# Performance work log

Hardware: AMD Instinct MI355X
Metric: run time of the kernel (lower is better)

Reference implementation:

```python
import jax, jax.numpy as jnp
import numpy as np

KSIZE = 51  # radius=50 is even -> incremented to 51 in __init__


def _gaussian_1d(ksize):
    # cv2.getGaussianKernel with sigma<=0: sigma = 0.3*((ksize-1)*0.5 - 1) + 0.8
    sigma = 0.3 * ((ksize - 1) * 0.5 - 1) + 0.8
    x = np.arange(ksize, dtype=np.float64) - (ksize - 1) / 2
    g = np.exp(-(x * x) / (2.0 * sigma * sigma))
    g = g / g.sum()
    return g.astype(np.float32)


def _blur(img, kernel1d):
    """Separable Gaussian blur with reflect padding.
    Mathematically identical to the 2D conv with outer(g, g) in the torch code.
    img: (b, c, h, w), kernel1d: (k,)
    """
    k = kernel1d.shape[0]
    p = k // 2
    b, c, h, w = img.shape
    x = jnp.pad(img, ((0, 0), (0, 0), (p, p), (p, p)), mode='reflect')
    x = x.reshape(b * c, 1, h + 2 * p, w + 2 * p)
    # vertical pass then horizontal pass (conv vs correlation irrelevant: symmetric kernel)
    kv = kernel1d.reshape(1, 1, k, 1)
    kh = kernel1d.reshape(1, 1, 1, k)
    dn = ('NCHW', 'OIHW', 'NCHW')
    x = jax.lax.conv_general_dilated(x, kv, (1, 1), 'VALID', dimension_numbers=dn)
    x = jax.lax.conv_general_dilated(x, kh, (1, 1), 'VALID', dimension_numbers=dn)
    return x.reshape(b, c, h, w)


def setup_inputs() -> dict:
    key = jax.random.key(0)
    img = jax.random.uniform(key, (16, 3, 512, 512), dtype=jnp.float32)
    kernel1d = jnp.asarray(_gaussian_1d(KSIZE))
    return {"img": img, "kernel1d": kernel1d}


def reference(img, kernel1d):
    weight = 0.5
    threshold = 10.0
    blur = _blur(img, kernel1d)
    residual = img - blur
    mask = (jnp.abs(residual) * 255.0 > threshold).astype(img.dtype)
    soft_mask = _blur(mask, kernel1d)
    sharp = jnp.clip(img + weight * residual, 0.0, 1.0)
    return soft_mask * sharp + (1.0 - soft_mask) * img
```

## Files before the change

kernel.cpp:

```cpp
#include <hip/hip_runtime.h>
#include <hip/hip_bf16.h>


typedef __attribute__((ext_vector_type(8))) short bf16x8;
typedef __attribute__((ext_vector_type(4))) float f32x4;

constexpr int IMG = 512, NIMG = 48, K = 51;
constexpr int SP = 136;
constexpr int YP = 136;
constexpr int SROWS = 128;
constexpr int SDATA = 122;

__device__ __forceinline__ float bf2f(unsigned short u) {
    return __builtin_bit_cast(float, (unsigned)u << 16);
}
__device__ __forceinline__ unsigned short f2bf(float f) {
    unsigned u = __builtin_bit_cast(unsigned, f);
    u += 0x7FFF + ((u >> 16) & 1);
    return (unsigned short)(u >> 16);
}
__device__ __forceinline__ int refl(int i) {
    i = i < 0 ? -i : i;
    return i >= IMG ? 2 * IMG - 2 - i : i;
}

template <int PASS>
__global__ __launch_bounds__(512, 6) void usm_kern(const float* __restrict__ img,
                                                   unsigned short* __restrict__ resbuf,
                                                   float* __restrict__ out,
                                                   const float* __restrict__ k1d) {
    __shared__ unsigned short st[SROWS * SP];
    __shared__ unsigned short Hl[64 * YP];

    const int tid = threadIdx.x, lane = tid & 63;
    const int wv = __builtin_amdgcn_readfirstlane(tid >> 6);
    const int m16 = lane & 15, g = lane >> 4;

    const int id = blockIdx.x;
    const int sw = (id & 7) * 384 + (id >> 3);
    const int bz = sw >> 6, r6 = sw & 63, byy = r6 >> 3, bxx = r6 & 7;
    const int x0 = bxx * 64, y0 = byy * 64;
    const size_t base = (size_t)bz * (IMG * IMG);

#pragma unroll
    for (int e = 0; e < 4; ++e) {
        const int idx = tid + e * 512;
        const int band = idx >> 10, rem = idx & 1023;
        const int mm = rem >> 6, kk = rem & 63;
        const int t = kk - mm + band;
        Hl[idx] = ((unsigned)t < (unsigned)K) ? f2bf(k1d[t]) : (unsigned short)0;
    }

    const bool xedge = (bxx == 0) | (bxx == 7);
    const int r0 = tid >> 4, c8 = (tid & 15) * 8;
#pragma unroll
    for (int j = 0; j < 4; ++j) {
        const int s = r0 + 32 * j;
        const int y = refl(y0 - 33 + min(s, SDATA - 1));
        const size_t rowb = base + (size_t)y * IMG;
        unsigned pk[4];
        if (PASS == 0) {
            float v[8];
            if (!xedge) {
                const f32x4 f0 = *(const f32x4*)&img[rowb + (x0 - 32 + c8)];
                const f32x4 f1 = *(const f32x4*)&img[rowb + (x0 - 32 + c8 + 4)];
#pragma unroll
                for (int e2 = 0; e2 < 4; ++e2) { v[e2] = f0[e2]; v[e2 + 4] = f1[e2]; }
            } else {
#pragma unroll
                for (int e2 = 0; e2 < 8; ++e2) v[e2] = img[rowb + refl(x0 - 32 + c8 + e2)];
            }
#pragma unroll
            for (int w = 0; w < 4; ++w)
                pk[w] = (unsigned)f2bf(v[2 * w]) | ((unsigned)f2bf(v[2 * w + 1]) << 16);
        } else {
            unsigned short u[8];
            if (!xedge) {
                const uint4 q4 = *(const uint4*)&resbuf[rowb + (x0 - 32 + c8)];
                const unsigned ww[4] = {q4.x, q4.y, q4.z, q4.w};
#pragma unroll
                for (int w = 0; w < 4; ++w) {
                    u[2 * w] = (unsigned short)ww[w];
                    u[2 * w + 1] = (unsigned short)(ww[w] >> 16);
                }
            } else {
#pragma unroll
                for (int e2 = 0; e2 < 8; ++e2) u[e2] = resbuf[rowb + refl(x0 - 32 + c8 + e2)];
            }
#pragma unroll
            for (int w = 0; w < 4; ++w) {
                const unsigned lo = ((u[2 * w]     & 0x7FFFu) > 0x3D20u) ? 0x3F80u : 0u;
                const unsigned hi = ((u[2 * w + 1] & 0x7FFFu) > 0x3D20u) ? 0x3F80u : 0u;
                pk[w] = lo | (hi << 16);
            }
        }
        *(uint4*)&st[s * SP + c8] = make_uint4(pk[0], pk[1], pk[2], pk[3]);
    }
    __syncthreads();

    bf16x8 a_v[2], a_h[2];
#pragma unroll
    for (int rs = 0; rs < 2; ++rs) {
        a_v[rs] = *(const bf16x8*)&Hl[m16 * 64 + rs * 32 + 8 * g];
        a_h[rs] = *(const bf16x8*)&Hl[1024 + m16 * 64 + rs * 32 + 8 * g];
    }
    const float gg0 = k1d[0], gg49 = k1d[49], gg50 = k1d[50];
    __syncthreads();

#pragma unroll
    for (int k4 = 0; k4 < 4; ++k4) {
        const int t = wv + 8 * k4;
        const int xs = t & 3, yt = t >> 2;
        const int n = 16 * yt + m16;
        f32x4 acc = {0.f, 0.f, 0.f, 0.f};
#pragma unroll
        for (int rs = 0; rs < 2; ++rs) {
            const bf16x8 b = *(const bf16x8*)&st[n * SP + 16 * xs + 8 + 32 * rs + 8 * g];
            acc = __builtin_amdgcn_mfma_f32_16x16x32_bf16(a_h[rs], b, acc, 0, 0, 0);
        }
        if (g == 0) acc[0] = fmaf(gg0,  bf2f(st[n * SP + 16 * xs + 7]),  acc[0]);
        if (g == 3) acc[3] = fmaf(gg50, bf2f(st[n * SP + 16 * xs + 72]), acc[3]);
#pragma unroll
        for (int q = 0; q < 4; ++q)
            Hl[(16 * xs + 4 * g + q) * YP + n] = f2bf(acc[q]);
    }
    __syncthreads();

#pragma unroll
    for (int k2 = 0; k2 < 2; ++k2) {
        const int t = wv + 8 * k2;
        const int xs2 = t & 3, ys = t >> 2;
        const int xl = 16 * xs2 + m16;
        f32x4 acc = {0.f, 0.f, 0.f, 0.f};
#pragma unroll
        for (int rs = 0; rs < 2; ++rs) {
            const bf16x8 b = *(const bf16x8*)&Hl[xl * YP + 16 * ys + 8 + 32 * rs + 8 * g];
            acc = __builtin_amdgcn_mfma_f32_16x16x32_bf16(a_v[rs], b, acc, 0, 0, 0);
        }
        if (g == 3) {
            const float h72 = bf2f(Hl[xl * YP + 16 * ys + 72]);
            const float h73 = bf2f(Hl[xl * YP + 16 * ys + 73]);
            acc[2] = fmaf(gg50, h72, acc[2]);
            acc[3] = fmaf(gg49, h72, fmaf(gg50, h73, acc[3]));
        }
        const int yl0 = 16 * ys + 4 * g;
#pragma unroll
        for (int q = 0; q < 4; ++q) {
            const size_t di = base + (size_t)(y0 + yl0 + q) * IMG + (x0 + xl);
            const float iv = img[di];
            if (PASS == 0) {
                resbuf[di] = f2bf(iv - acc[q]);
            } else {
                const float rv = bf2f(resbuf[di]);
                float sharp = fmaf(0.5f, rv, iv);
                sharp = fminf(fmaxf(sharp, 0.f), 1.f);
                out[di] = fmaf(acc[q], sharp - iv, iv);
            }
        }
    }
}

extern "C" void kernel_launch(void* const* d_in, const int* in_sizes, int n_in,
                              void* d_out, int out_size, void* d_ws, size_t ws_size,
                              hipStream_t stream) {
    (void)in_sizes; (void)n_in; (void)out_size; (void)ws_size;
    const float* img = (const float*)d_in[0];
    const float* k1d = (const float*)d_in[1];
    float* out = (float*)d_out;
    unsigned short* rs = (unsigned short*)d_ws;

    const dim3 grid(NIMG * 64);

    usm_kern<0><<<grid, 512, 0, stream>>>(img, rs, out, k1d);
    usm_kern<1><<<grid, 512, 0, stream>>>(img, rs, out, k1d);
}
```

Measured before the change: 103.6 us.

## Store byte mask in pass 0, build MFMA kernel fragments in registers

Pass 0 now computes the threshold mask from the fp32 residual and writes it as a separate byte buffer. Pass 1 reads that byte mask for its halo-heavy tile load instead of re-reading the bf16 residual and thresholding it. The banded Gaussian A-fragments are built directly in registers from k1d rather than staged through shared memory, which removes one barrier, and addressing switches to 32-bit offsets from per-image base pointers. The cost is an extra byte store per pixel in pass 0, and the mask now comes from the unrounded residual, so it can differ slightly from the old bf16-based threshold.

After: 98.33 us. 1.05x faster.

```diff
diff --git a/kernel.cpp b/kernel.cpp
--- a/kernel.cpp
+++ b/kernel.cpp
@@ -27,6 +27,7 @@
 template <int PASS>
 __global__ __launch_bounds__(512, 6) void usm_kern(const float* __restrict__ img,
                                                    unsigned short* __restrict__ resbuf,
+                                                   unsigned char* __restrict__ maskbuf,
                                                    float* __restrict__ out,
                                                    const float* __restrict__ k1d) {
     __shared__ unsigned short st[SROWS * SP];
@@ -41,70 +42,70 @@
     const int bz = sw >> 6, r6 = sw & 63, byy = r6 >> 3, bxx = r6 & 7;
     const int x0 = bxx * 64, y0 = byy * 64;
     const size_t base = (size_t)bz * (IMG * IMG);
+    const float* __restrict__ imgb = img + base;
+    unsigned short* __restrict__ resb = resbuf + base;
+    unsigned char* __restrict__ maskb = maskbuf + base;
+    float* __restrict__ outb = out + base;
 
+    bf16x8 a_v[2], a_h[2];
 #pragma unroll
-    for (int e = 0; e < 4; ++e) {
-        const int idx = tid + e * 512;
-        const int band = idx >> 10, rem = idx & 1023;
-        const int mm = rem >> 6, kk = rem & 63;
-        const int t = kk - mm + band;
-        Hl[idx] = ((unsigned)t < (unsigned)K) ? f2bf(k1d[t]) : (unsigned short)0;
+    for (int rs = 0; rs < 2; ++rs) {
+        float gt[9];
+#pragma unroll
+        for (int e = 0; e < 9; ++e) {
+            const int t = 32 * rs + 8 * g + e - m16;
+            gt[e] = ((unsigned)t < (unsigned)K) ? k1d[t] : 0.f;
+        }
+#pragma unroll
+        for (int j = 0; j < 8; ++j) {
+            a_v[rs][j] = (short)f2bf(gt[j]);
+            a_h[rs][j] = (short)f2bf(gt[j + 1]);
+        }
     }
+    const float gg0 = k1d[0], gg49 = k1d[49], gg50 = k1d[50];
 
     const bool xedge = (bxx == 0) | (bxx == 7);
-    const int r0 = tid >> 4, c8 = (tid & 15) * 8;
+    const int r0t = tid >> 4, c8 = (tid & 15) * 8;
 #pragma unroll
     for (int j = 0; j < 4; ++j) {
-        const int s = r0 + 32 * j;
-        const int y = refl(y0 - 33 + min(s, SDATA - 1));
-        const size_t rowb = base + (size_t)y * IMG;
+        const int s = r0t + 32 * j;
+        const int rowo = refl(y0 - 33 + min(s, SDATA - 1)) * IMG + (x0 - 32 + c8);
         unsigned pk[4];
         if (PASS == 0) {
             float v[8];
             if (!xedge) {
-                const f32x4 f0 = *(const f32x4*)&img[rowb + (x0 - 32 + c8)];
-                const f32x4 f1 = *(const f32x4*)&img[rowb + (x0 - 32 + c8 + 4)];
+                const f32x4 f0 = *(const f32x4*)&imgb[rowo];
+                const f32x4 f1 = *(const f32x4*)&imgb[rowo + 4];
 #pragma unroll
-                for (int e2 = 0; e2 < 4; ++e2) { v[e2] = f0[e2]; v[e2 + 4] = f1[e2]; }
+                for (int e = 0; e < 4; ++e) { v[e] = f0[e]; v[e + 4] = f1[e]; }
             } else {
+                const int rb = rowo - (x0 - 32 + c8);
 #pragma unroll
-                for (int e2 = 0; e2 < 8; ++e2) v[e2] = img[rowb + refl(x0 - 32 + c8 + e2)];
+                for (int e = 0; e < 8; ++e) v[e] = imgb[rb + refl(x0 - 32 + c8 + e)];
             }
 #pragma unroll
             for (int w = 0; w < 4; ++w)
                 pk[w] = (unsigned)f2bf(v[2 * w]) | ((unsigned)f2bf(v[2 * w + 1]) << 16);
         } else {
-            unsigned short u[8];
+            unsigned char mb[8];
             if (!xedge) {
-                const uint4 q4 = *(const uint4*)&resbuf[rowb + (x0 - 32 + c8)];
-                const unsigned ww[4] = {q4.x, q4.y, q4.z, q4.w};
+                const uint2 mv = *(const uint2*)&maskb[rowo];
 #pragma unroll
-                for (int w = 0; w < 4; ++w) {
-                    u[2 * w] = (unsigned short)ww[w];
-                    u[2 * w + 1] = (unsigned short)(ww[w] >> 16);
+                for (int e = 0; e < 4; ++e) {
+                    mb[e] = (unsigned char)(mv.x >> (8 * e));
+                    mb[e + 4] = (unsigned char)(mv.y >> (8 * e));
                 }
             } else {
+                const int rb = rowo - (x0 - 32 + c8);
 #pragma unroll
-                for (int e2 = 0; e2 < 8; ++e2) u[e2] = resbuf[rowb + refl(x0 - 32 + c8 + e2)];
+                for (int e = 0; e < 8; ++e) mb[e] = maskb[rb + refl(x0 - 32 + c8 + e)];
             }
 #pragma unroll
-            for (int w = 0; w < 4; ++w) {
-                const unsigned lo = ((u[2 * w]     & 0x7FFFu) > 0x3D20u) ? 0x3F80u : 0u;
-                const unsigned hi = ((u[2 * w + 1] & 0x7FFFu) > 0x3D20u) ? 0x3F80u : 0u;
-                pk[w] = lo | (hi << 16);
-            }
+            for (int w = 0; w < 4; ++w)
+                pk[w] = (mb[2 * w] ? 0x3F80u : 0u) | ((mb[2 * w + 1] ? 0x3F80u : 0u) << 16);
         }
         *(uint4*)&st[s * SP + c8] = make_uint4(pk[0], pk[1], pk[2], pk[3]);
     }
-    __syncthreads();
-
-    bf16x8 a_v[2], a_h[2];
-#pragma unroll
-    for (int rs = 0; rs < 2; ++rs) {
-        a_v[rs] = *(const bf16x8*)&Hl[m16 * 64 + rs * 32 + 8 * g];
-        a_h[rs] = *(const bf16x8*)&Hl[1024 + m16 * 64 + rs * 32 + 8 * g];
-    }
-    const float gg0 = k1d[0], gg49 = k1d[49], gg50 = k1d[50];
     __syncthreads();
 
 #pragma unroll
@@ -146,15 +147,17 @@
         const int yl0 = 16 * ys + 4 * g;
 #pragma unroll
         for (int q = 0; q < 4; ++q) {
-            const size_t di = base + (size_t)(y0 + yl0 + q) * IMG + (x0 + xl);
-            const float iv = img[di];
+            const int di = (y0 + yl0 + q) * IMG + (x0 + xl);
+            const float iv = imgb[di];
             if (PASS == 0) {
-                resbuf[di] = f2bf(iv - acc[q]);
+                const float rv = iv - acc[q];
+                resb[di] = f2bf(rv);
+                maskb[di] = (fabsf(rv) * 255.0f > 10.0f) ? 1 : 0;
             } else {
-                const float rv = bf2f(resbuf[di]);
+                const float rv = bf2f(resb[di]);
                 float sharp = fmaf(0.5f, rv, iv);
                 sharp = fminf(fmaxf(sharp, 0.f), 1.f);
-                out[di] = fmaf(acc[q], sharp - iv, iv);
+                outb[di] = fmaf(acc[q], sharp - iv, iv);
             }
         }
     }
@@ -168,9 +171,10 @@
     const float* k1d = (const float*)d_in[1];
     float* out = (float*)d_out;
     unsigned short* rs = (unsigned short*)d_ws;
+    unsigned char* mk = (unsigned char*)d_ws + (size_t)NIMG * IMG * IMG * 2;
 
     const dim3 grid(NIMG * 64);
 
-    usm_kern<0><<<grid, 512, 0, stream>>>(img, rs, out, k1d);
-    usm_kern<1><<<grid, 512, 0, stream>>>(img, rs, out, k1d);
+    usm_kern<0><<<grid, 512, 0, stream>>>(img, rs, mk, out, k1d);
+    usm_kern<1><<<grid, 512, 0, stream>>>(img, rs, mk, out, k1d);
 }
```
